# Kernel optimization log

Measured on AMD Instinct MI355X. Metric: run time of the kernel, lower is better.

Reference implementation:

```python
import jax, jax.numpy as jnp
import numpy as np

N1 = 4096
N2 = 4096


def _encoder(x, w1, b1, w2, b2, w3, b3):
    # fc1 -> fc2 -> fc3 -> relu (relu only after fc3, matching the torch code)
    h = x @ w1.T + b1
    h = h @ w2.T + b2
    h = h @ w3.T + b3
    return jax.nn.relu(h)


def _self_attention(x, adj, alpha, W):
    # tmp_i = sum_j [adj_ij==1] * alpha_ij * W * x_j ; tmp_i /= deg_i ; tmp_i += x_i (only if deg_i != 0)
    a = (adj == 1).astype(x.dtype)          # [N, N]
    deg = a.sum(axis=1)                     # [N]
    agg = (a * alpha) @ x                   # [N, 64] masked weighted aggregation
    agg = agg * W[0, 0]
    safe_deg = jnp.maximum(deg, 1.0)
    out = agg / safe_deg[:, None] + x       # residual
    return jnp.where((deg != 0.0)[:, None], out, jnp.zeros_like(out))


def setup_inputs() -> dict:
    key = jax.random.key(0)
    ks = jax.random.split(key, 20)
    s = 0.02  # weight scale to keep activations sane through the 4096->256->128->64 MLP
    inp = {
        "x1": jax.random.normal(ks[0], (N1, N1), jnp.float32),
        "x2": jax.random.normal(ks[1], (N2, N2), jnp.float32),
        "adj1": jax.random.randint(ks[2], (N1, N1), 0, 2, jnp.int32),
        "adj2": jax.random.randint(ks[3], (N2, N2), 0, 2, jnp.int32),
        "e1_w1": jax.random.normal(ks[4], (256, N1), jnp.float32) * s,
        "e1_b1": jnp.zeros((256,), jnp.float32),
        "e1_w2": jax.random.normal(ks[5], (128, 256), jnp.float32) * s,
        "e1_b2": jnp.zeros((128,), jnp.float32),
        "e1_w3": jax.random.normal(ks[6], (64, 128), jnp.float32) * s,
        "e1_b3": jnp.zeros((64,), jnp.float32),
        "e2_w1": jax.random.normal(ks[7], (256, N2), jnp.float32) * s,
        "e2_b1": jnp.zeros((256,), jnp.float32),
        "e2_w2": jax.random.normal(ks[8], (128, 256), jnp.float32) * s,
        "e2_b2": jnp.zeros((128,), jnp.float32),
        "e2_w3": jax.random.normal(ks[9], (64, 128), jnp.float32) * s,
        "e2_b3": jnp.zeros((64,), jnp.float32),
        "W": jax.random.normal(ks[10], (1, 1), jnp.float32),
        "alpha1": jax.random.normal(ks[11], (N1, N1), jnp.float32),
        "clf_w": jax.random.normal(ks[12], (2, (N1 + N2) * 64), jnp.float32) * s,
        "clf_b": jnp.zeros((2,), jnp.float32),
    }
    return inp


def reference(x1, x2, adj1, adj2,
              e1_w1, e1_b1, e1_w2, e1_b2, e1_w3, e1_b3,
              e2_w1, e2_b1, e2_w2, e2_b2, e2_w3, e2_b3,
              W, alpha1, clf_w, clf_b):
    h1 = _encoder(x1, e1_w1, e1_b1, e1_w2, e1_b2, e1_w3, e1_b3)  # [N1, 64]
    h2 = _encoder(x2, e2_w1, e2_b1, e2_w2, e2_b2, e2_w3, e2_b3)  # [N2, 64]
    # NOTE: original torch code uses self.alpha1 for BOTH graphs (alpha2 is unused)
    new1 = _self_attention(h1, adj1, alpha1, W)
    new2 = _self_attention(h2, adj2, alpha1[:N2, :N2], W)
    feat = jnp.concatenate([new1, new2], axis=0).reshape(1, -1)  # [1, (N1+N2)*64]
    return feat @ clf_w.T + clf_b  # [1, 2]
```

## Files before the change

kernel.cpp:

```cpp
#include <hip/hip_runtime.h>
#include <hip/hip_bf16.h>
#include <stdint.h>

#define N 4096

typedef __attribute__((ext_vector_type(4))) float f32x4;
typedef __attribute__((ext_vector_type(8))) short s16x8;

__device__ inline unsigned short f2bf(float f) {
    unsigned int u = __float_as_uint(f);
    u += 0x7fffu + ((u >> 16) & 1u);
    return (unsigned short)(u >> 16);
}
__device__ inline float bf2f(unsigned short h) {
    return __uint_as_float(((unsigned int)h) << 16);
}

__global__ void k0a(const float* __restrict__ w2a, const float* __restrict__ w3a,
                    const float* __restrict__ b1a, const float* __restrict__ b2a, const float* __restrict__ b3a,
                    const float* __restrict__ w2b, const float* __restrict__ w3b,
                    const float* __restrict__ b1b, const float* __restrict__ b2b, const float* __restrict__ b3b,
                    float* __restrict__ T, float* __restrict__ beff) {
    const int g  = blockIdx.x >> 5;
    const int nb = blockIdx.x & 31;
    const float* w2 = g ? w2b : w2a;
    const float* w3 = g ? w3b : w3a;
    const int c  = threadIdx.x;
    const int n0 = nb * 2;
    float a0 = 0.f, a1 = 0.f;
#pragma unroll 8
    for (int r = 0; r < 128; ++r) {
        float w = w2[r * 256 + c];
        a0 += w3[n0 * 128 + r] * w;
        a1 += w3[n0 * 128 + 128 + r] * w;
    }
    float* Tg = T + g * 64 * 256;
    Tg[n0 * 256 + c]       = a0;
    Tg[(n0 + 1) * 256 + c] = a1;

    if (nb == 0) {
        __shared__ float ps[256];
        __shared__ float u[128];
        const float* b1 = g ? b1b : b1a;
        const float* b2 = g ? b2b : b2a;
        const float* b3 = g ? b3b : b3a;
        {
            const int r = threadIdx.x >> 1, half = threadIdx.x & 1;
            float s = 0.f;
#pragma unroll 8
            for (int cc = 0; cc < 128; ++cc) s += w2[r * 256 + half * 128 + cc] * b1[half * 128 + cc];
            ps[threadIdx.x] = s;
        }
        __syncthreads();
        if (threadIdx.x < 128)
            u[threadIdx.x] = ps[2 * threadIdx.x] + ps[2 * threadIdx.x + 1] + b2[threadIdx.x];
        __syncthreads();
        {
            const int n = threadIdx.x >> 2, qr = threadIdx.x & 3;
            float s = 0.f;
#pragma unroll
            for (int r = 0; r < 32; ++r) s += w3[n * 128 + qr * 32 + r] * u[qr * 32 + r];
            ps[threadIdx.x] = s;
        }
        __syncthreads();
        if (threadIdx.x < 64)
            beff[g * 64 + threadIdx.x] = ps[4 * threadIdx.x] + ps[4 * threadIdx.x + 1]
                                       + ps[4 * threadIdx.x + 2] + ps[4 * threadIdx.x + 3] + b3[threadIdx.x];
    }
}

__global__ __launch_bounds__(256) void k0b(const float* __restrict__ w1a, const float* __restrict__ w1b,
                                           const float* __restrict__ T,
                                           unsigned short* __restrict__ Wfrag) {
    const int b  = blockIdx.x;
    const int g = b >> 8, n4 = (b >> 4) & 15, kchunk = b & 15;
    const float* w1 = g ? w1b : w1a;
    const int kx = kchunk * 256 + threadIdx.x;
    const float* Tg = T + (size_t)(g * 64 + n4 * 4) * 256;
    float acc[4] = {0.f, 0.f, 0.f, 0.f};
#pragma unroll 8
    for (int r = 0; r < 256; ++r) {
        float w = w1[(size_t)r * N + kx];
#pragma unroll
        for (int j = 0; j < 4; ++j) acc[j] += Tg[j * 256 + r] * w;
    }
    const int kc = kx >> 6, cc = (kx >> 5) & 1, q = (kx >> 3) & 3, ko = kx & 7;
#pragma unroll
    for (int j = 0; j < 4; ++j) {
        const int n = n4 * 4 + j;
        const int ng = n >> 4, l15 = n & 15;
        const int lane = q * 16 + l15;
        const unsigned short hi = f2bf(acc[j]);
        const unsigned short lo = f2bf(acc[j] - bf2f(hi));
        const size_t unit = ((((size_t)g * 64 + kc) * 4 + ng) * 2 + cc) * 2;
        Wfrag[unit * 512 + lane * 8 + ko]       = hi;
        Wfrag[(unit + 1) * 512 + lane * 8 + ko] = lo;
    }
}

__global__ __launch_bounds__(512, 2) void k1(const float* __restrict__ x1, const float* __restrict__ x2,
                                             const unsigned short* __restrict__ Wfrag,
                                             float* __restrict__ ph) {
    const int b  = blockIdx.x;
    const int rt = b >> 2, ks = b & 3;
    const int g  = rt >> 6;
    const int rbase = (rt & 63) * 64;
    const float* x = g ? x2 : x1;

    const int t = threadIdx.x;
    const int lane = t & 63, w = t >> 6;
    const int rg = w & 3, kh = w >> 2;
    const int q = lane >> 4, l15 = lane & 15;

    __shared__ float accs_h[4][4][64][4];

    f32x4 acc[4];
#pragma unroll
    for (int ng = 0; ng < 4; ++ng) acc[ng] = (f32x4){0.f, 0.f, 0.f, 0.f};

    const float* xrow = x + (size_t)(rbase + rg * 16 + l15) * N;
    const int kcbase = ks * 16 + kh * 8;

    float4 pa0, pa1, ra0, ra1;

#define K1_LOADX(A0, A1, IT) do { \
        const int kc_ = kcbase + ((IT) >> 1), c_ = (IT) & 1; \
        const int ka_ = kc_ * 64 + c_ * 32 + q * 8; \
        A0 = *(const float4*)&xrow[ka_]; \
        A1 = *(const float4*)&xrow[ka_ + 4]; \
    } while (0)

#define K1_STEP(A0, A1, IT) do { \
        const int kc_ = kcbase + ((IT) >> 1), c_ = (IT) & 1; \
        s16x8 bh[4], bl[4]; \
        _Pragma("unroll") \
        for (int ng = 0; ng < 4; ++ng) { \
            const size_t unit = ((((size_t)g * 64 + kc_) * 4 + ng) * 2 + c_) * 2; \
            bh[ng] = *(const s16x8*)&Wfrag[unit * 512 + lane * 8]; \
            bl[ng] = *(const s16x8*)&Wfrag[(unit + 1) * 512 + lane * 8]; \
        } \
        float xv[8] = {A0.x, A0.y, A0.z, A0.w, A1.x, A1.y, A1.z, A1.w}; \
        s16x8 ah, al; \
        _Pragma("unroll") \
        for (int j = 0; j < 8; ++j) { \
            unsigned short hh = f2bf(xv[j]); \
            ah[j] = (short)hh; \
            al[j] = (short)f2bf(xv[j] - bf2f(hh)); \
        } \
        _Pragma("unroll") \
        for (int ng = 0; ng < 4; ++ng) { \
            acc[ng] = __builtin_amdgcn_mfma_f32_16x16x32_bf16(al, bh[ng], acc[ng], 0, 0, 0); \
            acc[ng] = __builtin_amdgcn_mfma_f32_16x16x32_bf16(ah, bl[ng], acc[ng], 0, 0, 0); \
            acc[ng] = __builtin_amdgcn_mfma_f32_16x16x32_bf16(ah, bh[ng], acc[ng], 0, 0, 0); \
        } \
    } while (0)

    K1_LOADX(pa0, pa1, 0);
    __builtin_amdgcn_sched_barrier(0);
#pragma unroll
    for (int it2 = 0; it2 < 8; ++it2) {
        K1_LOADX(ra0, ra1, 2 * it2 + 1);
        __builtin_amdgcn_sched_barrier(0);
        K1_STEP(pa0, pa1, 2 * it2);
        if (it2 < 7) {
            K1_LOADX(pa0, pa1, 2 * it2 + 2);
            __builtin_amdgcn_sched_barrier(0);
        }
        K1_STEP(ra0, ra1, 2 * it2 + 1);
    }
#undef K1_LOADX
#undef K1_STEP

    if (kh == 1) {
#pragma unroll
        for (int ng = 0; ng < 4; ++ng)
#pragma unroll
            for (int r = 0; r < 4; ++r) accs_h[rg][ng][lane][r] = acc[ng][r];
    }
    __syncthreads();
    if (kh == 0) {
        const int girow = g * 4096 + rbase + rg * 16 + q * 4;
#pragma unroll
        for (int ng = 0; ng < 4; ++ng) {
            const int n = ng * 16 + l15;
#pragma unroll
            for (int r = 0; r < 4; ++r) {
                float s = acc[ng][r] + accs_h[rg][ng][lane][r];
                ph[((size_t)ks * 8192 + girow + r) * 64 + n] = s;
            }
        }
    }
}

__global__ __launch_bounds__(256) void k1b(const float* __restrict__ ph, const float* __restrict__ beff,
                                           float* __restrict__ hf, unsigned short* __restrict__ hfrag) {
    const int b = blockIdx.x;
    const int g = b & 1;
    const int i0 = (b >> 1) * 16;
    const int t = threadIdx.x;
    const int il = t >> 4, nq = t & 15;
    const int gi = g * 4096 + i0 + il;

    __shared__ unsigned short htile[64][16];

    f32x4 s = (f32x4){0.f, 0.f, 0.f, 0.f};
#pragma unroll
    for (int ks = 0; ks < 4; ++ks)
        s += *(const f32x4*)&ph[((size_t)ks * 8192 + gi) * 64 + nq * 4];
    f32x4 o;
#pragma unroll
    for (int j = 0; j < 4; ++j) {
        const int n = nq * 4 + j;
        float v = fmaxf(s[j] + beff[g * 64 + n], 0.f);
        o[j] = v;
        htile[n][il] = f2bf(v);
    }
    *(f32x4*)&hf[(size_t)gi * 64 + nq * 4] = o;
    __syncthreads();

    if (t < 128) {
        const int ng2 = t >> 5, jh = (t >> 4) & 1, l = t & 15;
        uint4 v = *(const uint4*)&htile[ng2 * 16 + l][jh * 8];
        const int jc = i0 >> 6, c = (i0 >> 5) & 1, q0 = (i0 >> 3) & 3;
        const size_t unit = (((size_t)g * 4 + ng2) * 64 + jc) * 2 + c;
        *(uint4*)&hfrag[unit * 512 + (size_t)(q0 + jh) * 128 + l * 8] = v;
    }
}

__global__ __launch_bounds__(512, 2) void k2(const int* __restrict__ adj1, const int* __restrict__ adj2,
                                             const float* __restrict__ alpha,
                                             const unsigned short* __restrict__ hfrag,
                                             float* __restrict__ pagg, float* __restrict__ pdeg) {
    const int b  = blockIdx.x;
    const int ks = (b >> 1) & 3;
    const int i0 = ((((b >> 3) << 1) | (b & 1))) << 4;
    const int t = threadIdx.x;
    const int lane = t & 63, kg = t >> 6;
    const int q = lane >> 4, l15 = lane & 15;

    __shared__ __align__(16) unsigned short am[2][2][16][256];
    __shared__ float degp[2][16][32];
    float (*accs)[4][64][4] = reinterpret_cast<float (*)[4][64][4]>(&am[0][0][0][0]);

    f32x4 acc1[4], acc2[4];
#pragma unroll
    for (int ng = 0; ng < 4; ++ng) {
        acc1[ng] = (f32x4){0.f, 0.f, 0.f, 0.f};
        acc2[ng] = (f32x4){0.f, 0.f, 0.f, 0.f};
    }
    int deg1 = 0, deg2 = 0;

    const int srow = t >> 5, scg = t & 31;
    const size_t sbase = (size_t)(i0 + srow) * N + (size_t)ks * 1024 + (size_t)scg * 8;
    char* const amb = (char*)&am[0][0][0][0];
    const int swoff = (srow * 512 + scg * 16) ^ ((srow & 7) << 4);
    const int rdoff = (l15 * 512 + kg * 64 + q * 16) ^ ((l15 & 7) << 4);

    float4 sa0, sa1; int4 sj10, sj11, sj20, sj21;

#define K2_ISSUE(S) do { \
        const float* ap = alpha + sbase + (S) * 256; \
        sa0 = *(const float4*)ap; sa1 = *(const float4*)(ap + 4); \
        const int* p1 = adj1 + sbase + (S) * 256; \
        sj10 = *(const int4*)p1; sj11 = *(const int4*)(p1 + 4); \
        const int* p2 = adj2 + sbase + (S) * 256; \
        sj20 = *(const int4*)p2; sj21 = *(const int4*)(p2 + 4); \
    } while (0)

#define K2_CONVSTORE(BUF) do { \
        float av[8] = {sa0.x, sa0.y, sa0.z, sa0.w, sa1.x, sa1.y, sa1.z, sa1.w}; \
        int m1[8] = {sj10.x == 1, sj10.y == 1, sj10.z == 1, sj10.w == 1, \
                     sj11.x == 1, sj11.y == 1, sj11.z == 1, sj11.w == 1}; \
        int m2[8] = {sj20.x == 1, sj20.y == 1, sj20.z == 1, sj20.w == 1, \
                     sj21.x == 1, sj21.y == 1, sj21.z == 1, sj21.w == 1}; \
        s16x8 w1v, w2v; \
        _Pragma("unroll") \
        for (int j = 0; j < 8; ++j) { \
            unsigned short bv = f2bf(av[j]); \
            w1v[j] = m1[j] ? (short)bv : (short)0; \
            w2v[j] = m2[j] ? (short)bv : (short)0; \
            deg1 += m1[j]; deg2 += m2[j]; \
        } \
        *(s16x8*)(amb + (BUF) * 16384 + swoff) = w1v; \
        *(s16x8*)(amb + (BUF) * 16384 + 8192 + swoff) = w2v; \
    } while (0)

#define K2_COMPUTE(S) do { \
        const int jc = ks * 16 + (S) * 4 + (kg >> 1), cph = kg & 1; \
        s16x8 ha1[4], ha2[4]; \
        _Pragma("unroll") \
        for (int ng = 0; ng < 4; ++ng) { \
            const size_t u1 = (((size_t)ng) * 64 + jc) * 2 + cph; \
            const size_t u2 = (((size_t)(4 + ng)) * 64 + jc) * 2 + cph; \
            ha1[ng] = *(const s16x8*)&hfrag[u1 * 512 + lane * 8]; \
            ha2[ng] = *(const s16x8*)&hfrag[u2 * 512 + lane * 8]; \
        } \
        s16x8 bfa = *(const s16x8*)(amb + ((S) & 1) * 16384 + rdoff); \
        s16x8 bfb = *(const s16x8*)(amb + ((S) & 1) * 16384 + 8192 + rdoff); \
        _Pragma("unroll") \
        for (int ng = 0; ng < 4; ++ng) { \
            acc1[ng] = __builtin_amdgcn_mfma_f32_16x16x32_bf16(ha1[ng], bfa, acc1[ng], 0, 0, 0); \
            acc2[ng] = __builtin_amdgcn_mfma_f32_16x16x32_bf16(ha2[ng], bfb, acc2[ng], 0, 0, 0); \
        } \
    } while (0)

    K2_ISSUE(0);
    K2_CONVSTORE(0);
    __syncthreads();
#pragma unroll
    for (int s = 0; s < 4; ++s) {
        if (s < 3) K2_ISSUE(s + 1);
        K2_COMPUTE(s);
        if (s < 3) K2_CONVSTORE((s + 1) & 1);
        __syncthreads();
    }

    degp[0][srow][scg] = (float)deg1;
    degp[1][srow][scg] = (float)deg2;
#pragma unroll
    for (int ng = 0; ng < 4; ++ng)
#pragma unroll
        for (int r = 0; r < 4; ++r) accs[kg][ng][lane][r] = acc1[ng][r];
    __syncthreads();
    if (t < 32) {
        const int gg = t >> 4, row = t & 15;
        float s = 0.f;
#pragma unroll
        for (int c2 = 0; c2 < 32; ++c2) s += degp[gg][row][c2];
        pdeg[(size_t)(gg * 4 + ks) * 4096 + i0 + row] = s;
    }

    {
        const int ng = kg & 3, rh = kg >> 2;
        const int i = i0 + l15;
#pragma unroll
        for (int rr = 0; rr < 2; ++rr) {
            const int r = rh * 2 + rr;
            float s = 0.f;
#pragma unroll
            for (int k8 = 0; k8 < 8; ++k8) s += accs[k8][ng][lane][r];
            const int n = ng * 16 + q * 4 + r;
            pagg[(((size_t)ks * 4096 + i) << 6) + n] = s;
        }
    }
    __syncthreads();
#pragma unroll
    for (int ng = 0; ng < 4; ++ng)
#pragma unroll
        for (int r = 0; r < 4; ++r) accs[kg][ng][lane][r] = acc2[ng][r];
    __syncthreads();
    {
        const int ng = kg & 3, rh = kg >> 2;
        const int i = i0 + l15;
#pragma unroll
        for (int rr = 0; rr < 2; ++rr) {
            const int r = rh * 2 + rr;
            float s = 0.f;
#pragma unroll
            for (int k8 = 0; k8 < 8; ++k8) s += accs[k8][ng][lane][r];
            const int n = ng * 16 + q * 4 + r;
            pagg[(((size_t)(4 + ks) * 4096 + i) << 6) + n] = s;
        }
    }
#undef K2_ISSUE
#undef K2_CONVSTORE
#undef K2_COMPUTE
}

__global__ __launch_bounds__(256) void k2b(const float* __restrict__ pagg, const float* __restrict__ pdeg,
                                           const float* __restrict__ hf, const float* __restrict__ Wp,
                                           float* __restrict__ outv) {
    const int idx = blockIdx.x * 256 + threadIdx.x;
    const int gi  = idx >> 4;
    const int nq  = idx & 15;
    const int g   = gi >> 12, i = gi & 4095;
    const float W00 = Wp[0];

    float dg = 0.f;
#pragma unroll
    for (int ks = 0; ks < 4; ++ks) dg += pdeg[(size_t)(g * 4 + ks) * 4096 + i];

    f32x4 s = (f32x4){0.f, 0.f, 0.f, 0.f};
#pragma unroll
    for (int ks = 0; ks < 4; ++ks) {
        const f32x4 p = *(const f32x4*)&pagg[(((size_t)(g * 4 + ks) * 4096 + i) << 6) + nq * 4];
        s += p;
    }
    const f32x4 hv = *(const f32x4*)&hf[((size_t)gi << 6) + nq * 4];
    const float dmax = fmaxf(dg, 1.f);
    f32x4 o;
#pragma unroll
    for (int j = 0; j < 4; ++j)
        o[j] = (dg != 0.f) ? (s[j] * W00 / dmax + hv[j]) : 0.f;
    *(f32x4*)&outv[((size_t)gi << 6) + nq * 4] = o;
}

__global__ __launch_bounds__(256) void k3a(const float* __restrict__ feat, const float* __restrict__ clfw,
                                           float* __restrict__ part) {
    const int t = threadIdx.x;
    const size_t idx = (size_t)blockIdx.x * 2048 + (size_t)t * 8;
    float4 a0 = *(const float4*)&feat[idx];
    float4 a1 = *(const float4*)&feat[idx + 4];
    float4 c0 = *(const float4*)&clfw[idx];
    float4 c1 = *(const float4*)&clfw[idx + 4];
    float4 d0 = *(const float4*)&clfw[524288 + idx];
    float4 d1 = *(const float4*)&clfw[524288 + idx + 4];
    float s0 = a0.x * c0.x + a0.y * c0.y + a0.z * c0.z + a0.w * c0.w
             + a1.x * c1.x + a1.y * c1.y + a1.z * c1.z + a1.w * c1.w;
    float s1 = a0.x * d0.x + a0.y * d0.y + a0.z * d0.z + a0.w * d0.w
             + a1.x * d1.x + a1.y * d1.y + a1.z * d1.z + a1.w * d1.w;
    __shared__ float r0[256], r1[256];
    r0[t] = s0; r1[t] = s1;
    __syncthreads();
    for (int s = 128; s > 0; s >>= 1) {
        if (t < s) { r0[t] += r0[t + s]; r1[t] += r1[t + s]; }
        __syncthreads();
    }
    if (t == 0) { part[blockIdx.x * 2] = r0[0]; part[blockIdx.x * 2 + 1] = r1[0]; }
}

__global__ void k3b(const float* __restrict__ part, const float* __restrict__ clfb,
                    float* __restrict__ outp) {
    const int t = threadIdx.x;
    __shared__ float r0[256], r1[256];
    r0[t] = part[t * 2]; r1[t] = part[t * 2 + 1];
    __syncthreads();
    for (int s = 128; s > 0; s >>= 1) {
        if (t < s) { r0[t] += r0[t + s]; r1[t] += r1[t + s]; }
        __syncthreads();
    }
    if (t == 0) { outp[0] = r0[0] + clfb[0]; outp[1] = r1[0] + clfb[1]; }
}

extern "C" void kernel_launch(void* const* d_in, const int* in_sizes, int n_in,
                              void* d_out, int out_size, void* d_ws, size_t ws_size,
                              hipStream_t stream) {
    const float* x1   = (const float*)d_in[0];
    const float* x2   = (const float*)d_in[1];
    const int*   adj1 = (const int*)d_in[2];
    const int*   adj2 = (const int*)d_in[3];
    const float* e1w1 = (const float*)d_in[4];
    const float* e1b1 = (const float*)d_in[5];
    const float* e1w2 = (const float*)d_in[6];
    const float* e1b2 = (const float*)d_in[7];
    const float* e1w3 = (const float*)d_in[8];
    const float* e1b3 = (const float*)d_in[9];
    const float* e2w1 = (const float*)d_in[10];
    const float* e2b1 = (const float*)d_in[11];
    const float* e2w2 = (const float*)d_in[12];
    const float* e2b2 = (const float*)d_in[13];
    const float* e2w3 = (const float*)d_in[14];
    const float* e2b3 = (const float*)d_in[15];
    const float* Wp   = (const float*)d_in[16];
    const float* alph = (const float*)d_in[17];
    const float* clfw = (const float*)d_in[18];
    const float* clfb = (const float*)d_in[19];

    char* wsb = (char*)d_ws;
    unsigned short* Wfrag = (unsigned short*)(wsb);
    float* newv = (float*)(wsb);
    unsigned short* hfrag = (unsigned short*)(wsb + (2u << 20));
    float* hf   = (float*)(wsb + (3u << 20));
    float* T    = (float*)(wsb + (5u << 20));
    float* beff = (float*)(wsb + (5u << 20) + (1u << 17));
    float* part = (float*)(wsb + (5u << 20) + (1u << 17) + 4096);
    float* pagg = (float*)(wsb + (6u << 20));
    float* ph   = (float*)(wsb + (6u << 20));
    float* pdeg = (float*)(wsb + (14u << 20));

    hipLaunchKernelGGL(k0a, dim3(64), dim3(256), 0, stream,
                       e1w2, e1w3, e1b1, e1b2, e1b3, e2w2, e2w3, e2b1, e2b2, e2b3, T, beff);
    hipLaunchKernelGGL(k0b, dim3(512), dim3(256), 0, stream, e1w1, e2w1, T, Wfrag);
    hipLaunchKernelGGL(k1, dim3(512), dim3(512), 0, stream, x1, x2, Wfrag, ph);
    hipLaunchKernelGGL(k1b, dim3(512), dim3(256), 0, stream, ph, beff, hf, hfrag);
    hipLaunchKernelGGL(k2, dim3(1024), dim3(512), 0, stream, adj1, adj2, alph, hfrag, pagg, pdeg);
    hipLaunchKernelGGL(k2b, dim3(512), dim3(256), 0, stream, pagg, pdeg, hf, Wp, newv);
    hipLaunchKernelGGL(k3a, dim3(256), dim3(256), 0, stream, newv, clfw, part);
    hipLaunchKernelGGL(k3b, dim3(1), dim3(256), 0, stream, part, clfb, (float*)d_out);
}
```

Baseline: 388.9 us.

## Pack adjacency into bitmasks early and fuse finalize with classifier

Extra blocks added to k0b convert each int32 adjacency matrix into a packed 1-bit mask and compute the row degrees there. k2 then reads one mask byte per 8 entries instead of two int4 pairs, which cuts its global traffic for adj1 and adj2. Separately, the residual/normalize kernel is fused with the classifier dot-product partial reduction, so the intermediate feature vector is never written out and one launch is dropped. The full adjacency read still happens, now in k0b, and the workspace buffers are laid out again to make room for the masks.

```diff
diff --git a/kernel.cpp b/kernel.cpp
--- a/kernel.cpp
+++ b/kernel.cpp
@@ -71,8 +71,43 @@
 
 __global__ __launch_bounds__(256) void k0b(const float* __restrict__ w1a, const float* __restrict__ w1b,
                                            const float* __restrict__ T,
-                                           unsigned short* __restrict__ Wfrag) {
+                                           unsigned short* __restrict__ Wfrag,
+                                           const int* __restrict__ adj1, const int* __restrict__ adj2,
+                                           uint8_t* __restrict__ mask1, uint8_t* __restrict__ mask2,
+                                           float* __restrict__ pdeg) {
+    __shared__ float pcs[4][64];
     const int b  = blockIdx.x;
+    if (b >= 512) {
+        const int pb = b - 512;
+        const int g = pb >> 10;
+        const int rowblk = pb & 1023;
+        const int* adj = g ? adj2 : adj1;
+        uint8_t* mask  = g ? mask2 : mask1;
+        const int r = threadIdx.x >> 6;
+        const int lane = threadIdx.x & 63;
+        const int row = rowblk * 4 + r;
+        const int* src = adj + (size_t)row * N + lane * 64;
+        unsigned long long bits = 0ull;
+#pragma unroll
+        for (int i = 0; i < 64; i += 4) {
+            int4 v = *(const int4*)&src[i];
+            bits |= ((unsigned long long)(v.x == 1)) << i;
+            bits |= ((unsigned long long)(v.y == 1)) << (i + 1);
+            bits |= ((unsigned long long)(v.z == 1)) << (i + 2);
+            bits |= ((unsigned long long)(v.w == 1)) << (i + 3);
+        }
+        *(unsigned long long*)&mask[(size_t)row * 512 + lane * 8] = bits;
+        pcs[r][lane] = (float)__popcll(bits);
+        __syncthreads();
+        if (threadIdx.x < 16) {
+            const int rr = threadIdx.x >> 2, ksq = threadIdx.x & 3;
+            float s = 0.f;
+#pragma unroll
+            for (int u = 0; u < 16; ++u) s += pcs[rr][ksq * 16 + u];
+            pdeg[(size_t)(g * 4 + ksq) * 4096 + rowblk * 4 + rr] = s;
+        }
+        return;
+    }
     const int g = b >> 8, n4 = (b >> 4) & 15, kchunk = b & 15;
     const float* w1 = g ? w1b : w1a;
     const int kx = kchunk * 256 + threadIdx.x;
@@ -227,10 +262,10 @@
     }
 }
 
-__global__ __launch_bounds__(512, 2) void k2(const int* __restrict__ adj1, const int* __restrict__ adj2,
+__global__ __launch_bounds__(512, 2) void k2(const uint8_t* __restrict__ mask1, const uint8_t* __restrict__ mask2,
                                              const float* __restrict__ alpha,
                                              const unsigned short* __restrict__ hfrag,
-                                             float* __restrict__ pagg, float* __restrict__ pdeg) {
+                                             float* __restrict__ pagg) {
     const int b  = blockIdx.x;
     const int ks = (b >> 1) & 3;
     const int i0 = ((((b >> 3) << 1) | (b & 1))) << 4;
@@ -239,7 +274,6 @@
     const int q = lane >> 4, l15 = lane & 15;
 
     __shared__ __align__(16) unsigned short am[2][2][16][256];
-    __shared__ float degp[2][16][32];
     float (*accs)[4][64][4] = reinterpret_cast<float (*)[4][64][4]>(&am[0][0][0][0]);
 
     f32x4 acc1[4], acc2[4];
@@ -248,38 +282,31 @@
         acc1[ng] = (f32x4){0.f, 0.f, 0.f, 0.f};
         acc2[ng] = (f32x4){0.f, 0.f, 0.f, 0.f};
     }
-    int deg1 = 0, deg2 = 0;
 
     const int srow = t >> 5, scg = t & 31;
     const size_t sbase = (size_t)(i0 + srow) * N + (size_t)ks * 1024 + (size_t)scg * 8;
+    const size_t mbase = (size_t)(i0 + srow) * 512 + (size_t)ks * 128 + (size_t)scg;
     char* const amb = (char*)&am[0][0][0][0];
     const int swoff = (srow * 512 + scg * 16) ^ ((srow & 7) << 4);
     const int rdoff = (l15 * 512 + kg * 64 + q * 16) ^ ((l15 & 7) << 4);
 
-    float4 sa0, sa1; int4 sj10, sj11, sj20, sj21;
+    float4 sa0, sa1; unsigned sm1, sm2;
 
 #define K2_ISSUE(S) do { \
         const float* ap = alpha + sbase + (S) * 256; \
         sa0 = *(const float4*)ap; sa1 = *(const float4*)(ap + 4); \
-        const int* p1 = adj1 + sbase + (S) * 256; \
-        sj10 = *(const int4*)p1; sj11 = *(const int4*)(p1 + 4); \
-        const int* p2 = adj2 + sbase + (S) * 256; \
-        sj20 = *(const int4*)p2; sj21 = *(const int4*)(p2 + 4); \
+        sm1 = mask1[mbase + (S) * 32]; \
+        sm2 = mask2[mbase + (S) * 32]; \
     } while (0)
 
 #define K2_CONVSTORE(BUF) do { \
         float av[8] = {sa0.x, sa0.y, sa0.z, sa0.w, sa1.x, sa1.y, sa1.z, sa1.w}; \
-        int m1[8] = {sj10.x == 1, sj10.y == 1, sj10.z == 1, sj10.w == 1, \
-                     sj11.x == 1, sj11.y == 1, sj11.z == 1, sj11.w == 1}; \
-        int m2[8] = {sj20.x == 1, sj20.y == 1, sj20.z == 1, sj20.w == 1, \
-                     sj21.x == 1, sj21.y == 1, sj21.z == 1, sj21.w == 1}; \
         s16x8 w1v, w2v; \
         _Pragma("unroll") \
         for (int j = 0; j < 8; ++j) { \
             unsigned short bv = f2bf(av[j]); \
-            w1v[j] = m1[j] ? (short)bv : (short)0; \
-            w2v[j] = m2[j] ? (short)bv : (short)0; \
-            deg1 += m1[j]; deg2 += m2[j]; \
+            w1v[j] = ((sm1 >> j) & 1u) ? (short)bv : (short)0; \
+            w2v[j] = ((sm2 >> j) & 1u) ? (short)bv : (short)0; \
         } \
         *(s16x8*)(amb + (BUF) * 16384 + swoff) = w1v; \
         *(s16x8*)(amb + (BUF) * 16384 + 8192 + swoff) = w2v; \
@@ -315,21 +342,11 @@
         __syncthreads();
     }
 
-    degp[0][srow][scg] = (float)deg1;
-    degp[1][srow][scg] = (float)deg2;
 #pragma unroll
     for (int ng = 0; ng < 4; ++ng)
 #pragma unroll
         for (int r = 0; r < 4; ++r) accs[kg][ng][lane][r] = acc1[ng][r];
     __syncthreads();
-    if (t < 32) {
-        const int gg = t >> 4, row = t & 15;
-        float s = 0.f;
-#pragma unroll
-        for (int c2 = 0; c2 < 32; ++c2) s += degp[gg][row][c2];
-        pdeg[(size_t)(gg * 4 + ks) * 4096 + i0 + row] = s;
-    }
-
     {
         const int ng = kg & 3, rh = kg >> 2;
         const int i = i0 + l15;
@@ -367,9 +384,9 @@
 #undef K2_COMPUTE
 }
 
-__global__ __launch_bounds__(256) void k2b(const float* __restrict__ pagg, const float* __restrict__ pdeg,
+__global__ __launch_bounds__(256) void k2c(const float* __restrict__ pagg, const float* __restrict__ pdeg,
                                            const float* __restrict__ hf, const float* __restrict__ Wp,
-                                           float* __restrict__ outv) {
+                                           const float* __restrict__ clfw, float* __restrict__ part) {
     const int idx = blockIdx.x * 256 + threadIdx.x;
     const int gi  = idx >> 4;
     const int nq  = idx & 15;
@@ -392,28 +409,18 @@
 #pragma unroll
     for (int j = 0; j < 4; ++j)
         o[j] = (dg != 0.f) ? (s[j] * W00 / dmax + hv[j]) : 0.f;
-    *(f32x4*)&outv[((size_t)gi << 6) + nq * 4] = o;
-}
-
-__global__ __launch_bounds__(256) void k3a(const float* __restrict__ feat, const float* __restrict__ clfw,
-                                           float* __restrict__ part) {
+
+    const float4 c0 = *(const float4*)&clfw[(size_t)idx * 4];
+    const float4 c1 = *(const float4*)&clfw[524288 + (size_t)idx * 4];
+    float s0 = o[0] * c0.x + o[1] * c0.y + o[2] * c0.z + o[3] * c0.w;
+    float s1 = o[0] * c1.x + o[1] * c1.y + o[2] * c1.z + o[3] * c1.w;
+
+    __shared__ float r0[256], r1[256];
     const int t = threadIdx.x;
-    const size_t idx = (size_t)blockIdx.x * 2048 + (size_t)t * 8;
-    float4 a0 = *(const float4*)&feat[idx];
-    float4 a1 = *(const float4*)&feat[idx + 4];
-    float4 c0 = *(const float4*)&clfw[idx];
-    float4 c1 = *(const float4*)&clfw[idx + 4];
-    float4 d0 = *(const float4*)&clfw[524288 + idx];
-    float4 d1 = *(const float4*)&clfw[524288 + idx + 4];
-    float s0 = a0.x * c0.x + a0.y * c0.y + a0.z * c0.z + a0.w * c0.w
-             + a1.x * c1.x + a1.y * c1.y + a1.z * c1.z + a1.w * c1.w;
-    float s1 = a0.x * d0.x + a0.y * d0.y + a0.z * d0.z + a0.w * d0.w
-             + a1.x * d1.x + a1.y * d1.y + a1.z * d1.z + a1.w * d1.w;
-    __shared__ float r0[256], r1[256];
     r0[t] = s0; r1[t] = s1;
     __syncthreads();
-    for (int s = 128; s > 0; s >>= 1) {
-        if (t < s) { r0[t] += r0[t + s]; r1[t] += r1[t + s]; }
+    for (int st = 128; st > 0; st >>= 1) {
+        if (t < st) { r0[t] += r0[t + st]; r1[t] += r1[t + st]; }
         __syncthreads();
     }
     if (t == 0) { part[blockIdx.x * 2] = r0[0]; part[blockIdx.x * 2 + 1] = r1[0]; }
@@ -423,7 +430,8 @@
                     float* __restrict__ outp) {
     const int t = threadIdx.x;
     __shared__ float r0[256], r1[256];
-    r0[t] = part[t * 2]; r1[t] = part[t * 2 + 1];
+    r0[t] = part[t * 2] + part[(t + 256) * 2];
+    r1[t] = part[t * 2 + 1] + part[(t + 256) * 2 + 1];
     __syncthreads();
     for (int s = 128; s > 0; s >>= 1) {
         if (t < s) { r0[t] += r0[t + s]; r1[t] += r1[t + s]; }
@@ -458,23 +466,24 @@
 
     char* wsb = (char*)d_ws;
     unsigned short* Wfrag = (unsigned short*)(wsb);
-    float* newv = (float*)(wsb);
+    float* hf   = (float*)(wsb);
     unsigned short* hfrag = (unsigned short*)(wsb + (2u << 20));
-    float* hf   = (float*)(wsb + (3u << 20));
-    float* T    = (float*)(wsb + (5u << 20));
-    float* beff = (float*)(wsb + (5u << 20) + (1u << 17));
-    float* part = (float*)(wsb + (5u << 20) + (1u << 17) + 4096);
-    float* pagg = (float*)(wsb + (6u << 20));
-    float* ph   = (float*)(wsb + (6u << 20));
-    float* pdeg = (float*)(wsb + (14u << 20));
+    uint8_t* mask1 = (uint8_t*)(wsb + (3u << 20));
+    uint8_t* mask2 = (uint8_t*)(wsb + (5u << 20));
+    float* pagg = (float*)(wsb + (7u << 20));
+    float* ph   = (float*)(wsb + (7u << 20));
+    float* pdeg = (float*)(wsb + (15u << 20));
+    float* T    = (float*)(wsb + (15u << 20) + (1u << 17));
+    float* beff = (float*)(wsb + (15u << 20) + (2u << 17));
+    float* part = (float*)(wsb + (15u << 20) + (2u << 17) + 4096);
 
     hipLaunchKernelGGL(k0a, dim3(64), dim3(256), 0, stream,
                        e1w2, e1w3, e1b1, e1b2, e1b3, e2w2, e2w3, e2b1, e2b2, e2b3, T, beff);
-    hipLaunchKernelGGL(k0b, dim3(512), dim3(256), 0, stream, e1w1, e2w1, T, Wfrag);
+    hipLaunchKernelGGL(k0b, dim3(2560), dim3(256), 0, stream, e1w1, e2w1, T, Wfrag,
+                       adj1, adj2, mask1, mask2, pdeg);
     hipLaunchKernelGGL(k1, dim3(512), dim3(512), 0, stream, x1, x2, Wfrag, ph);
     hipLaunchKernelGGL(k1b, dim3(512), dim3(256), 0, stream, ph, beff, hf, hfrag);
-    hipLaunchKernelGGL(k2, dim3(1024), dim3(512), 0, stream, adj1, adj2, alph, hfrag, pagg, pdeg);
-    hipLaunchKernelGGL(k2b, dim3(512), dim3(256), 0, stream, pagg, pdeg, hf, Wp, newv);
-    hipLaunchKernelGGL(k3a, dim3(256), dim3(256), 0, stream, newv, clfw, part);
+    hipLaunchKernelGGL(k2, dim3(1024), dim3(512), 0, stream, mask1, mask2, alph, hfrag, pagg);
+    hipLaunchKernelGGL(k2c, dim3(512), dim3(256), 0, stream, pagg, pdeg, hf, Wp, clfw, part);
     hipLaunchKernelGGL(k3b, dim3(1), dim3(256), 0, stream, part, clfb, (float*)d_out);
 }
```

New measurement: 393.3 us. About the same (+1.1%).
